# Kernel optimization log

Hardware: AMD Instinct MI355X
Metric: run time of the kernel (lower is better)

## Reference

```python
import math
import jax, jax.numpy as jnp
import numpy as np

B_IN, B_OUT = 32, 16
BATCH, F_IN, F_OUT = 16, 16, 64
N_ALPHA, N_BETA = 8, 4
MAX_BETA = math.pi / 8


def _wigner_d(l, betas):
    """d^l_{m',m}(beta) = <m'|exp(-i beta J_y)|m>, m ordered -l..l (quantum/CS convention)."""
    betas = np.asarray(betas, dtype=np.float64)
    if l == 0:
        return np.ones((len(betas), 1, 1))
    m = np.arange(-l, l)
    c = np.sqrt(l * (l + 1.0) - m * (m + 1.0))
    Jy = np.zeros((2 * l + 1, 2 * l + 1), dtype=np.complex128)
    i = np.arange(2 * l)
    Jy[i + 1, i] = c / 2j
    Jy[i, i + 1] = -c / 2j
    w, V = np.linalg.eigh(Jy)
    ph = np.exp(-1j * betas[:, None] * w[None, :])  # [nb, 2l+1]
    return np.einsum('mk,bk,nk->bmn', V, ph, V.conj()).real


def _quad_weights(b):
    # Driscoll-Healy quadrature weights for the 2b-point SOFT beta grid, incl. alpha weight 2pi/(2b)
    j = np.arange(2 * b)
    beta = np.pi * (2 * j + 1) / (4 * b)
    k = np.arange(b)
    s = np.sum(np.sin(beta[:, None] * (2 * k + 1)[None, :]) / (2 * k + 1)[None, :], axis=1)
    return (2.0 / b) * np.sin(beta) * s * (2.0 * np.pi / (2 * b))


def _tables():
    # S2 forward-FFT table: quadrature-weighted d^l_{m,0}(beta_j)
    betas_in = np.pi * (2 * np.arange(2 * B_IN) + 1) / (4 * B_IN)
    qw = _quad_weights(B_IN)
    nspec = B_OUT ** 2
    wig_s2 = np.zeros((2 * B_IN, nspec))
    for l in range(B_OUT):
        d = _wigner_d(l, betas_in)[:, :, l]  # d^l_{m,0}(beta_j), [2b_in, 2l+1]
        wig_s2[:, l * l:l * l + 2 * l + 1] = d * qw[:, None]
    # kernel spectral basis sampled on the (beta, alpha) grid: e^{-i m alpha} d^l_{m,0}(beta)
    gb = np.repeat((np.arange(N_BETA) + 1) * MAX_BETA / N_BETA, N_ALPHA)
    ga = np.tile(np.linspace(0, 2 * np.pi, N_ALPHA, endpoint=False), N_BETA)
    Fk = np.zeros((nspec, N_ALPHA * N_BETA), dtype=np.complex128)
    for l in range(B_OUT):
        d = _wigner_d(l, gb)[:, :, l]  # [n_grid, 2l+1]
        m = np.arange(-l, l + 1)
        Fk[l * l:l * l + 2 * l + 1] = np.exp(-1j * m[:, None] * ga[None, :]) * d.T
    # SO3 inverse-FFT table: (2l+1) * d^l_{m,n}(beta_k) on the output beta grid
    betas_out = np.pi * (2 * np.arange(2 * B_OUT) + 1) / (4 * B_OUT)
    nspec3 = sum((2 * l + 1) ** 2 for l in range(B_OUT))
    wig_so3 = np.zeros((2 * B_OUT, nspec3))
    off = 0
    for l in range(B_OUT):
        d = _wigner_d(l, betas_out)  # [2b_out, L, L]
        wig_so3[:, off:off + (2 * l + 1) ** 2] = (2 * l + 1) * d.reshape(2 * B_OUT, -1)
        off += (2 * l + 1) ** 2
    return wig_s2, Fk, wig_so3


def setup_inputs() -> dict:
    key = jax.random.key(0)
    kx, kk = jax.random.split(key)
    wig_s2, Fk, wig_so3 = _tables()
    return {
        "x": jax.random.normal(kx, (BATCH, F_IN, 2 * B_IN, 2 * B_IN), dtype=jnp.float32),
        "kernel": jax.random.uniform(kk, (F_IN, F_OUT, N_ALPHA * N_BETA), dtype=jnp.float32, minval=-1.0, maxval=1.0),
        "bias": jnp.zeros((1, F_OUT, 1, 1, 1), dtype=jnp.float32),
        "wig_s2": jnp.asarray(wig_s2, dtype=jnp.float32),
        "fk_re": jnp.asarray(Fk.real, dtype=jnp.float32),
        "fk_im": jnp.asarray(Fk.imag, dtype=jnp.float32),
        "wig_so3": jnp.asarray(wig_so3, dtype=jnp.float32),
    }


def reference(x, kernel, bias, wig_s2, fk_re, fk_im, wig_so3):
    b_in = x.shape[-1] // 2
    nspec = wig_s2.shape[1]
    b_out = int(round(math.sqrt(nspec)))
    batch, f_in = x.shape[0], x.shape[1]
    f_out, n_grid = kernel.shape[1], kernel.shape[2]
    scaling = 1.0 / math.sqrt(n_grid * f_in * b_out ** 4.0 / b_in ** 2.0)

    # --- S2 FFT: FFT over alpha, then quadrature-weighted Legendre (Wigner d_{m0}) sum over beta ---
    xf = jnp.fft.fft(x.astype(jnp.complex64), axis=-1)  # [B, Fin, 2b_in(beta), m-bins]
    m_idx = np.concatenate([np.arange(-l, l + 1) % (2 * b_in) for l in range(b_out)])  # ragged l*m layout
    fhat = jnp.einsum('bfjs,js->sbf', xf[:, :, :, m_idx], wig_s2.astype(jnp.complex64))  # [nspec, B, Fin]

    # --- s2_rft: kernel -> spherical-harmonic coefficients on the sampling grid ---
    Fk = jax.lax.complex(fk_re, fk_im)  # [nspec, n_grid]
    psi = jnp.einsum('iog,sg->sio', (kernel * scaling).astype(jnp.complex64), Fk)  # [nspec, Fin, Fout]

    # --- s2_mm (per-degree ragged block outer product) + SO3 inverse FFT ---
    spec = jnp.zeros((batch, f_out, 2 * b_out, 2 * b_out, 2 * b_out), dtype=jnp.complex64)
    off = 0
    for l in range(b_out):
        L = 2 * l + 1
        s = slice(l * l, l * l + L)
        # Fz^l_{mn} = sum_i fhat^l_m[b,i] * conj(psi^l_n[i,o])
        Fz = jnp.einsum('mbi,nio->bomn', fhat[s], jnp.conj(psi[s]))  # [B, Fout, L, L]
        d_l = wig_so3[:, off:off + L * L].reshape(2 * b_out, L, L).astype(jnp.complex64)
        mi = np.arange(-l, l + 1) % (2 * b_out)
        spec = spec.at[:, :, :, mi[:, None], mi[None, :]].add(
            jnp.einsum('bomn,kmn->bokmn', Fz, d_l))
        off += L * L
    # inverse 2D FFT over (m->alpha, n->gamma); 'forward' norm = unnormalized synthesis sum
    out = jnp.fft.ifft2(spec, axes=(-2, -1), norm='forward').real  # [B, Fout, beta, alpha, gamma]
    return out + bias
```

## Files before the change

### kernel.cpp

```cpp
#include <hip/hip_runtime.h>
#include <math.h>

#define BATCH  16
#define F_IN   16
#define F_OUT  64
#define NGRID  32
#define NSPEC  256
#define NU     136
#define NITEMS 496
#define NP     2856
#define SCALING 0.005524271728019903f
#define PI_F 3.14159265358979323846f
#define W32 0.19634954084936207f

__device__ const int d_cof2[16] = {0,5,22,59,124,225,370,567,824,1149,1550,2035,2612,3289,4074,4975};
__device__ const int d_cumO[16] = {0,16,91,217,386,590,821,1071,1332,1596,1855,2101,2326,2522,2681,2795};

__device__ __forceinline__ void decode_p(int p, int& l, int& m, int& n, int& lam) {
    int L = 0;
    #pragma unroll
    for (int q = 1; q < 16; ++q) if (p >= d_cumO[q]) L = q;
    const int len = 16 - L;
    int q = p - d_cumO[L];
    int ti = (int)((float)q * (1.0f / (float)len));
    int r = q - ti * len;
    if (r < 0) { ti--; r += len; }
    else if (r >= len) { ti++; r -= len; }
    l = L + r;
    lam = L;
    if (ti < 2 * L + 1) { m = L; n = ti - L; }
    else { const int r2 = ti - (2 * L + 1); m = r2 >> 1; n = (r2 & 1) ? L : -L; }
}

__global__ __launch_bounds__(256) void k0_wigt(const float* __restrict__ wig,
                                               float* __restrict__ wigt) {
    const int t = blockIdx.x * 256 + threadIdx.x;
    if (t >= NP * 8) return;
    const int p = t >> 3, kq = t & 7;
    int l, m, n, lam;
    decode_p(p, l, m, n, lam);
    const int wo = d_cof2[l] + m * (2 * l + 1) + n;
    float4 v;
    v.x = wig[(kq * 4 + 0) * 5456 + wo];
    v.y = wig[(kq * 4 + 1) * 5456 + wo];
    v.z = wig[(kq * 4 + 2) * 5456 + wo];
    v.w = wig[(kq * 4 + 3) * 5456 + wo];
    *((float4*)(wigt + ((size_t)kq * NP + p) * 4)) = v;
}

__global__ __launch_bounds__(256) void k1_fhat(const float* __restrict__ x,
                                               const float* __restrict__ wig_s2,
                                               float2* __restrict__ fhat) {
    __shared__ float  xs[64][65];
    __shared__ float2 xf[16][65];
    const int b = blockIdx.x >> 4, f = blockIdx.x & 15;
    const int tid = threadIdx.x;

    const float4* src = (const float4*)(x + (size_t)(b * F_IN + f) * 4096);
    for (int t = tid; t < 1024; t += 256) {
        float4 v = src[t];
        const int row = t >> 4, col = (t & 15) * 4;
        xs[row][col] = v.x; xs[row][col+1] = v.y; xs[row][col+2] = v.z; xs[row][col+3] = v.w;
    }
    __syncthreads();

    {
        const int m = tid >> 4, j0 = tid & 15;
        float stc, sts;
        sincosf(-(2.f * PI_F / 64.f) * (float)m, &sts, &stc);
        float wr = 1.f, wi = 0.f;
        float ar[4] = {0,0,0,0}, ai[4] = {0,0,0,0};
        #pragma unroll 8
        for (int a = 0; a < 64; ++a) {
            #pragma unroll
            for (int q = 0; q < 4; ++q) {
                const float v = xs[j0 + 16*q][a];
                ar[q] += v * wr; ai[q] += v * wi;
            }
            const float nr = wr*stc - wi*sts; wi = wr*sts + wi*stc; wr = nr;
        }
        #pragma unroll
        for (int q = 0; q < 4; ++q) xf[m][j0 + 16*q] = make_float2(ar[q], ai[q]);
    }
    __syncthreads();

    if (tid < NU) {
        int l = (int)((sqrtf(8.f * (float)tid + 1.f) - 1.f) * 0.5f);
        while ((l + 1) * (l + 2) / 2 <= tid) ++l;
        while (l * (l + 1) / 2 > tid) --l;
        const int m = tid - l * (l + 1) / 2;
        const int s = l * l + l + m;
        float re = 0.f, im = 0.f;
        #pragma unroll 8
        for (int j = 0; j < 64; ++j) {
            const float2 v = xf[m][j];
            const float w = wig_s2[j * NSPEC + s];
            re += v.x * w; im += v.y * w;
        }
        fhat[(b * NU + tid) * F_IN + f] = make_float2(re, im);
    }
}

__global__ __launch_bounds__(256) void k2_psic(const float* __restrict__ kern,
                                               const float* __restrict__ fk_re,
                                               const float* __restrict__ fk_im,
                                               float2* __restrict__ psic) {
    __shared__ float2 fk[NGRID];
    const int s = blockIdx.x;
    const int tid = threadIdx.x;
    if (tid < NGRID) fk[tid] = make_float2(fk_re[s * NGRID + tid], -fk_im[s * NGRID + tid]);
    __syncthreads();
    for (int t = tid; t < F_OUT * F_IN; t += 256) {
        const int o = t >> 4, i = t & 15;
        const float* kr = kern + (size_t)(i * F_OUT + o) * NGRID;
        float re = 0.f, im = 0.f;
        for (int g = 0; g < NGRID; ++g) {
            const float v = kr[g];
            re += v * fk[g].x;
            im += v * fk[g].y;
        }
        psic[(o * NSPEC + s) * F_IN + i] = make_float2(re * SCALING, im * SCALING);
    }
}

__global__ __launch_bounds__(256) void k3a_fz(const float2* __restrict__ fhat,
                                              const float2* __restrict__ psic,
                                              float2* __restrict__ fzp) {
    __shared__ __align__(16) float2 fh[NU][18];
    __shared__ __align__(16) float2 ps[NSPEC][18];
    const int bo = blockIdx.x;
    const int b = bo >> 6, o = bo & 63;
    const int tid = threadIdx.x;

    {
        const float2* src = fhat + (size_t)b * NU * F_IN;
        for (int t = tid; t < NU * F_IN; t += 256) fh[t >> 4][t & 15] = src[t];
        const float2* src2 = psic + (size_t)o * NSPEC * F_IN;
        for (int t = tid; t < NSPEC * F_IN; t += 256) ps[t >> 4][t & 15] = src2[t];
    }
    __syncthreads();

    float2* dst = fzp + (size_t)bo * NP;
    for (int p = tid; p < NP; p += 256) {
        int l, m, n, lam;
        decode_p(p, l, m, n, lam);
        const int u = l * (l + 1) / 2 + m;
        const int sn = l * l + l + n;
        const float4* A4 = (const float4*)&fh[u][0];
        const float4* C4 = (const float4*)&ps[sn][0];
        float re = 0.f, im = 0.f;
        #pragma unroll
        for (int i2 = 0; i2 < 8; ++i2) {
            const float4 A = A4[i2], C = C4[i2];
            re += A.x*C.x - A.y*C.y + A.z*C.z - A.w*C.w;
            im += A.x*C.y + A.y*C.x + A.z*C.w + A.w*C.z;
        }
        dst[p] = make_float2(re, im);
    }
}

__global__ __launch_bounds__(256) void k3c_main(const float2* __restrict__ fzp,
                                               const float* __restrict__ wigt,
                                               const float* __restrict__ bias,
                                               float* __restrict__ out) {
    __shared__ __align__(16) float2 S[4][16][33];
    __shared__ __align__(16) float2 G[4][16][33];
    __shared__ float2 tw[32];
    const int bo = blockIdx.x >> 3;
    const int kc = blockIdx.x & 7;
    const int tid = threadIdx.x;
    const float bb = bias[bo & 63];

    if (tid < 32) {
        float s_, c_;
        sincosf(W32 * (float)tid, &s_, &c_);
        tw[tid] = make_float2(c_, s_);
    }

    const float2* fzb = fzp + (size_t)bo * NP;
    const float4* wtb = (const float4*)wigt + (size_t)kc * NP;

    #pragma unroll
    for (int it = 0; it < 2; ++it) {
        const int t = tid + it * 256;
        if (t < NITEMS) {
            int lam = (int)sqrtf((float)t * 0.5f);
            while ((2*lam + 1) * (lam + 1) <= t) ++lam;
            while (lam > 0 && (2*lam - 1) * lam > t) --lam;
            const int r = t - (2*lam - 1) * lam;
            int m, n;
            if (r < 2*lam + 1) { m = lam; n = r - lam; }
            else { const int r2 = r - (2*lam + 1); m = r2 >> 1; n = (r2 & 1) ? lam : -lam; }
            const int len = 16 - lam;
            const int O = d_cumO[lam] + r * len;
            const float2* fz = fzb + O;
            const float4* wt = wtb + O;
            float sr0=0,si0=0,sr1=0,si1=0,sr2=0,si2=0,sr3=0,si3=0;
            for (int j = 0; j < len; ++j) {
                const float2 z = fz[j];
                const float4 w = wt[j];
                sr0 += z.x * w.x; si0 += z.y * w.x;
                sr1 += z.x * w.y; si1 += z.y * w.y;
                sr2 += z.x * w.z; si2 += z.y * w.z;
                sr3 += z.x * w.w; si3 += z.y * w.w;
            }
            const int nn = n + 15;
            S[0][m][nn] = make_float2(sr0, si0);
            S[1][m][nn] = make_float2(sr1, si1);
            S[2][m][nn] = make_float2(sr2, si2);
            S[3][m][nn] = make_float2(sr3, si3);
        }
    }
    __syncthreads();

    {
        const int kk = tid >> 6, m = (tid >> 2) & 15, g0 = tid & 3;
        float ar[4] = {0,0,0,0}, ai[4] = {0,0,0,0}, br[4] = {0,0,0,0}, bi[4] = {0,0,0,0};
        const float2* Srow = &S[kk][m][0];
        #pragma unroll
        for (int nn = 0; nn < 31; ++nn) {
            const float2 sv = Srow[nn];
            const int n = nn - 15;
            #pragma unroll
            for (int q = 0; q < 4; ++q) {
                const int g = g0 + 4 * q;
                const float2 w = tw[(n * g) & 31];
                const float X = sv.x * w.x - sv.y * w.y;
                const float Y = sv.x * w.y + sv.y * w.x;
                ar[q] += X; ai[q] += Y;
                if (nn & 1) { br[q] += X; bi[q] += Y; }
                else        { br[q] -= X; bi[q] -= Y; }
            }
        }
        #pragma unroll
        for (int q = 0; q < 4; ++q) {
            const int g = g0 + 4 * q;
            G[kk][m][g]      = make_float2(ar[q], ai[q]);
            G[kk][m][g + 16] = make_float2(br[q], bi[q]);
        }
    }
    __syncthreads();

    float* outs = (float*)&S[0][0][0];
    {
        const int kk = tid >> 6, g = tid & 31, a0 = (tid >> 5) & 1;
        const float base = G[kk][0][g].x + bb;
        float o_[4][4];
        #pragma unroll
        for (int rep = 0; rep < 4; ++rep)
            #pragma unroll
            for (int j = 0; j < 4; ++j) o_[rep][j] = base;
        #pragma unroll
        for (int m = 1; m < 16; ++m) {
            const float2 gv = G[kk][m][g];
            const float gx = 2.f * gv.x, gy = 2.f * gv.y;
            #pragma unroll
            for (int rep = 0; rep < 4; ++rep) {
                const int A = a0 + 2 * rep;
                const float2 w = tw[(m * A) & 31];
                const float X = gx * w.x - gy * w.y;
                const float Y = gx * w.y + gy * w.x;
                o_[rep][0] += X;
                o_[rep][1] += ((m & 3) == 1) ? -Y : ((m & 3) == 2) ? -X : ((m & 3) == 3) ? Y : X;
                o_[rep][2] += (m & 1) ? -X : X;
                o_[rep][3] += ((m & 3) == 1) ? Y : ((m & 3) == 2) ? -X : ((m & 3) == 3) ? -Y : X;
            }
        }
        #pragma unroll
        for (int rep = 0; rep < 4; ++rep) {
            #pragma unroll
            for (int j = 0; j < 4; ++j) {
                const int a = a0 + 2*rep + 8*j;
                outs[kk * 1024 + (a << 5) + g] = o_[rep][j];
            }
        }
    }
    __syncthreads();

    {
        const int k0 = kc * 4;
        float4* dst = (float4*)(out + (((size_t)bo << 15) + ((size_t)k0 << 10)));
        const float4* s4 = (const float4*)outs;
        #pragma unroll
        for (int it = 0; it < 4; ++it) dst[tid + it * 256] = s4[tid + it * 256];
    }
}

extern "C" void kernel_launch(void* const* d_in, const int* in_sizes, int n_in,
                              void* d_out, int out_size, void* d_ws, size_t ws_size,
                              hipStream_t stream) {
    const float* x       = (const float*)d_in[0];
    const float* kern    = (const float*)d_in[1];
    const float* bias    = (const float*)d_in[2];
    const float* wig_s2  = (const float*)d_in[3];
    const float* fk_re   = (const float*)d_in[4];
    const float* fk_im   = (const float*)d_in[5];
    const float* wig_so3 = (const float*)d_in[6];
    float* out = (float*)d_out;

    float2* fhat_t = (float2*)d_ws;
    float2* psic_t = (float2*)((char*)d_ws + 327680);
    float*  wigt   = (float*)((char*)d_ws + 2424832);
    float2* fzp    = (float2*)((char*)d_ws + 2790400);

    k0_wigt<<<(NP * 8 + 255) / 256, 256, 0, stream>>>(wig_so3, wigt);
    k1_fhat<<<BATCH * F_IN, 256, 0, stream>>>(x, wig_s2, fhat_t);
    k2_psic<<<NSPEC, 256, 0, stream>>>(kern, fk_re, fk_im, psic_t);
    k3a_fz<<<BATCH * F_OUT, 256, 0, stream>>>(fhat_t, psic_t, fzp);
    k3c_main<<<BATCH * F_OUT * 8, 256, 0, stream>>>(fzp, wigt, bias, out);
}
```

Baseline: 352.6 us.

## Merge prep kernels into one launch and halve beta slab per main block

```diff
diff --git a/kernel.cpp b/kernel.cpp
--- a/kernel.cpp
+++ b/kernel.cpp
@@ -32,94 +32,95 @@
     else { const int r2 = ti - (2 * L + 1); m = r2 >> 1; n = (r2 & 1) ? L : -L; }
 }
 
-__global__ __launch_bounds__(256) void k0_wigt(const float* __restrict__ wig,
-                                               float* __restrict__ wigt) {
-    const int t = blockIdx.x * 256 + threadIdx.x;
-    if (t >= NP * 8) return;
-    const int p = t >> 3, kq = t & 7;
-    int l, m, n, lam;
-    decode_p(p, l, m, n, lam);
-    const int wo = d_cof2[l] + m * (2 * l + 1) + n;
-    float4 v;
-    v.x = wig[(kq * 4 + 0) * 5456 + wo];
-    v.y = wig[(kq * 4 + 1) * 5456 + wo];
-    v.z = wig[(kq * 4 + 2) * 5456 + wo];
-    v.w = wig[(kq * 4 + 3) * 5456 + wo];
-    *((float4*)(wigt + ((size_t)kq * NP + p) * 4)) = v;
-}
-
-__global__ __launch_bounds__(256) void k1_fhat(const float* __restrict__ x,
-                                               const float* __restrict__ wig_s2,
-                                               float2* __restrict__ fhat) {
-    __shared__ float  xs[64][65];
-    __shared__ float2 xf[16][65];
-    const int b = blockIdx.x >> 4, f = blockIdx.x & 15;
+__global__ __launch_bounds__(256) void k_prep(const float* __restrict__ x,
+                                              const float* __restrict__ wig_s2,
+                                              const float* __restrict__ kern,
+                                              const float* __restrict__ fk_re,
+                                              const float* __restrict__ fk_im,
+                                              const float* __restrict__ wig,
+                                              float2* __restrict__ fhat,
+                                              float2* __restrict__ psic,
+                                              float2* __restrict__ wigt2) {
+    __shared__ __align__(16) char smem[25088];
+    const int blk = blockIdx.x;
     const int tid = threadIdx.x;
 
-    const float4* src = (const float4*)(x + (size_t)(b * F_IN + f) * 4096);
-    for (int t = tid; t < 1024; t += 256) {
-        float4 v = src[t];
-        const int row = t >> 4, col = (t & 15) * 4;
-        xs[row][col] = v.x; xs[row][col+1] = v.y; xs[row][col+2] = v.z; xs[row][col+3] = v.w;
-    }
-    __syncthreads();
-
-    {
-        const int m = tid >> 4, j0 = tid & 15;
-        float stc, sts;
-        sincosf(-(2.f * PI_F / 64.f) * (float)m, &sts, &stc);
-        float wr = 1.f, wi = 0.f;
-        float ar[4] = {0,0,0,0}, ai[4] = {0,0,0,0};
-        #pragma unroll 8
-        for (int a = 0; a < 64; ++a) {
-            #pragma unroll
-            for (int q = 0; q < 4; ++q) {
-                const float v = xs[j0 + 16*q][a];
-                ar[q] += v * wr; ai[q] += v * wi;
-            }
-            const float nr = wr*stc - wi*sts; wi = wr*sts + wi*stc; wr = nr;
-        }
-        #pragma unroll
-        for (int q = 0; q < 4; ++q) xf[m][j0 + 16*q] = make_float2(ar[q], ai[q]);
-    }
-    __syncthreads();
-
-    if (tid < NU) {
-        int l = (int)((sqrtf(8.f * (float)tid + 1.f) - 1.f) * 0.5f);
-        while ((l + 1) * (l + 2) / 2 <= tid) ++l;
-        while (l * (l + 1) / 2 > tid) --l;
-        const int m = tid - l * (l + 1) / 2;
-        const int s = l * l + l + m;
-        float re = 0.f, im = 0.f;
-        #pragma unroll 8
-        for (int j = 0; j < 64; ++j) {
-            const float2 v = xf[m][j];
-            const float w = wig_s2[j * NSPEC + s];
-            re += v.x * w; im += v.y * w;
-        }
-        fhat[(b * NU + tid) * F_IN + f] = make_float2(re, im);
-    }
-}
-
-__global__ __launch_bounds__(256) void k2_psic(const float* __restrict__ kern,
-                                               const float* __restrict__ fk_re,
-                                               const float* __restrict__ fk_im,
-                                               float2* __restrict__ psic) {
-    __shared__ float2 fk[NGRID];
-    const int s = blockIdx.x;
-    const int tid = threadIdx.x;
-    if (tid < NGRID) fk[tid] = make_float2(fk_re[s * NGRID + tid], -fk_im[s * NGRID + tid]);
-    __syncthreads();
-    for (int t = tid; t < F_OUT * F_IN; t += 256) {
-        const int o = t >> 4, i = t & 15;
-        const float* kr = kern + (size_t)(i * F_OUT + o) * NGRID;
-        float re = 0.f, im = 0.f;
-        for (int g = 0; g < NGRID; ++g) {
-            const float v = kr[g];
-            re += v * fk[g].x;
-            im += v * fk[g].y;
-        }
-        psic[(o * NSPEC + s) * F_IN + i] = make_float2(re * SCALING, im * SCALING);
+    if (blk < 256) {
+        float (*xs)[65]  = (float (*)[65])smem;
+        float2 (*xf)[65] = (float2 (*)[65])(smem + 16640);
+        const int b = blk >> 4, f = blk & 15;
+
+        const float4* src = (const float4*)(x + (size_t)(b * F_IN + f) * 4096);
+        for (int t = tid; t < 1024; t += 256) {
+            float4 v = src[t];
+            const int row = t >> 4, col = (t & 15) * 4;
+            xs[row][col] = v.x; xs[row][col+1] = v.y; xs[row][col+2] = v.z; xs[row][col+3] = v.w;
+        }
+        __syncthreads();
+        {
+            const int m = tid >> 4, j0 = tid & 15;
+            float stc, sts;
+            sincosf(-(2.f * PI_F / 64.f) * (float)m, &sts, &stc);
+            float wr = 1.f, wi = 0.f;
+            float ar[4] = {0,0,0,0}, ai[4] = {0,0,0,0};
+            #pragma unroll 8
+            for (int a = 0; a < 64; ++a) {
+                #pragma unroll
+                for (int q = 0; q < 4; ++q) {
+                    const float v = xs[j0 + 16*q][a];
+                    ar[q] += v * wr; ai[q] += v * wi;
+                }
+                const float nr = wr*stc - wi*sts; wi = wr*sts + wi*stc; wr = nr;
+            }
+            #pragma unroll
+            for (int q = 0; q < 4; ++q) xf[m][j0 + 16*q] = make_float2(ar[q], ai[q]);
+        }
+        __syncthreads();
+        if (tid < NU) {
+            int l = (int)((sqrtf(8.f * (float)tid + 1.f) - 1.f) * 0.5f);
+            while ((l + 1) * (l + 2) / 2 <= tid) ++l;
+            while (l * (l + 1) / 2 > tid) --l;
+            const int m = tid - l * (l + 1) / 2;
+            const int s = l * l + l + m;
+            float re = 0.f, im = 0.f;
+            #pragma unroll 8
+            for (int j = 0; j < 64; ++j) {
+                const float2 v = xf[m][j];
+                const float w = wig_s2[j * NSPEC + s];
+                re += v.x * w; im += v.y * w;
+            }
+            fhat[(b * NU + tid) * F_IN + f] = make_float2(re, im);
+        }
+    } else if (blk < 512) {
+        float2* fk = (float2*)smem;
+        const int s = blk - 256;
+        if (tid < NGRID) fk[tid] = make_float2(fk_re[s * NGRID + tid], -fk_im[s * NGRID + tid]);
+        __syncthreads();
+        for (int t = tid; t < F_OUT * F_IN; t += 256) {
+            const int o = t >> 4, i = t & 15;
+            const float4* kr = (const float4*)(kern + (size_t)(i * F_OUT + o) * NGRID);
+            float re = 0.f, im = 0.f;
+            #pragma unroll
+            for (int g4 = 0; g4 < 8; ++g4) {
+                const float4 v = kr[g4];
+                const float2 a = fk[g4*4+0], b2 = fk[g4*4+1], c = fk[g4*4+2], d = fk[g4*4+3];
+                re += v.x * a.x + v.y * b2.x + v.z * c.x + v.w * d.x;
+                im += v.x * a.y + v.y * b2.y + v.z * c.y + v.w * d.y;
+            }
+            psic[(o * NSPEC + s) * F_IN + i] = make_float2(re * SCALING, im * SCALING);
+        }
+    } else {
+        const int t = (blk - 512) * 256 + tid;
+        if (t < NP * 16) {
+            const int p = t >> 4, kp = t & 15;
+            int l, m, n, lam;
+            decode_p(p, l, m, n, lam);
+            const int wo = d_cof2[l] + m * (2 * l + 1) + n;
+            float2 v;
+            v.x = wig[(2 * kp + 0) * 5456 + wo];
+            v.y = wig[(2 * kp + 1) * 5456 + wo];
+            wigt2[(size_t)kp * NP + p] = v;
+        }
     }
 }
 
@@ -160,14 +161,14 @@
 }
 
 __global__ __launch_bounds__(256) void k3c_main(const float2* __restrict__ fzp,
-                                               const float* __restrict__ wigt,
+                                               const float2* __restrict__ wigt2,
                                                const float* __restrict__ bias,
                                                float* __restrict__ out) {
-    __shared__ __align__(16) float2 S[4][16][33];
-    __shared__ __align__(16) float2 G[4][16][33];
+    __shared__ __align__(16) float2 S[2][16][33];
+    __shared__ __align__(16) float2 G[2][16][33];
     __shared__ float2 tw[32];
-    const int bo = blockIdx.x >> 3;
-    const int kc = blockIdx.x & 7;
+    const int bo = blockIdx.x >> 4;
+    const int kc = blockIdx.x & 15;
     const int tid = threadIdx.x;
     const float bb = bias[bo & 63];
 
@@ -178,7 +179,7 @@
     }
 
     const float2* fzb = fzp + (size_t)bo * NP;
-    const float4* wtb = (const float4*)wigt + (size_t)kc * NP;
+    const float2* wtb = wigt2 + (size_t)kc * NP;
 
     #pragma unroll
     for (int it = 0; it < 2; ++it) {
@@ -194,36 +195,32 @@
             const int len = 16 - lam;
             const int O = d_cumO[lam] + r * len;
             const float2* fz = fzb + O;
-            const float4* wt = wtb + O;
-            float sr0=0,si0=0,sr1=0,si1=0,sr2=0,si2=0,sr3=0,si3=0;
+            const float2* wt = wtb + O;
+            float sr0=0,si0=0,sr1=0,si1=0;
             for (int j = 0; j < len; ++j) {
                 const float2 z = fz[j];
-                const float4 w = wt[j];
+                const float2 w = wt[j];
                 sr0 += z.x * w.x; si0 += z.y * w.x;
                 sr1 += z.x * w.y; si1 += z.y * w.y;
-                sr2 += z.x * w.z; si2 += z.y * w.z;
-                sr3 += z.x * w.w; si3 += z.y * w.w;
             }
             const int nn = n + 15;
             S[0][m][nn] = make_float2(sr0, si0);
             S[1][m][nn] = make_float2(sr1, si1);
-            S[2][m][nn] = make_float2(sr2, si2);
-            S[3][m][nn] = make_float2(sr3, si3);
         }
     }
     __syncthreads();
 
     {
-        const int kk = tid >> 6, m = (tid >> 2) & 15, g0 = tid & 3;
-        float ar[4] = {0,0,0,0}, ai[4] = {0,0,0,0}, br[4] = {0,0,0,0}, bi[4] = {0,0,0,0};
+        const int kk = tid >> 7, m = (tid >> 3) & 15, g0 = tid & 7;
+        float ar[2] = {0,0}, ai[2] = {0,0}, br[2] = {0,0}, bi[2] = {0,0};
         const float2* Srow = &S[kk][m][0];
         #pragma unroll
         for (int nn = 0; nn < 31; ++nn) {
             const float2 sv = Srow[nn];
             const int n = nn - 15;
             #pragma unroll
-            for (int q = 0; q < 4; ++q) {
-                const int g = g0 + 4 * q;
+            for (int q = 0; q < 2; ++q) {
+                const int g = g0 + 8 * q;
                 const float2 w = tw[(n * g) & 31];
                 const float X = sv.x * w.x - sv.y * w.y;
                 const float Y = sv.x * w.y + sv.y * w.x;
@@ -233,8 +230,8 @@
             }
         }
         #pragma unroll
-        for (int q = 0; q < 4; ++q) {
-            const int g = g0 + 4 * q;
+        for (int q = 0; q < 2; ++q) {
+            const int g = g0 + 8 * q;
             G[kk][m][g]      = make_float2(ar[q], ai[q]);
             G[kk][m][g + 16] = make_float2(br[q], bi[q]);
         }
@@ -243,11 +240,11 @@
 
     float* outs = (float*)&S[0][0][0];
     {
-        const int kk = tid >> 6, g = tid & 31, a0 = (tid >> 5) & 1;
+        const int kk = tid >> 7, g = tid & 31, a0 = (tid >> 5) & 3;
         const float base = G[kk][0][g].x + bb;
-        float o_[4][4];
-        #pragma unroll
-        for (int rep = 0; rep < 4; ++rep)
+        float o_[2][4];
+        #pragma unroll
+        for (int rep = 0; rep < 2; ++rep)
             #pragma unroll
             for (int j = 0; j < 4; ++j) o_[rep][j] = base;
         #pragma unroll
@@ -255,8 +252,8 @@
             const float2 gv = G[kk][m][g];
             const float gx = 2.f * gv.x, gy = 2.f * gv.y;
             #pragma unroll
-            for (int rep = 0; rep < 4; ++rep) {
-                const int A = a0 + 2 * rep;
+            for (int rep = 0; rep < 2; ++rep) {
+                const int A = a0 + 4 * rep;
                 const float2 w = tw[(m * A) & 31];
                 const float X = gx * w.x - gy * w.y;
                 const float Y = gx * w.y + gy * w.x;
@@ -267,10 +264,10 @@
             }
         }
         #pragma unroll
-        for (int rep = 0; rep < 4; ++rep) {
+        for (int rep = 0; rep < 2; ++rep) {
             #pragma unroll
             for (int j = 0; j < 4; ++j) {
-                const int a = a0 + 2*rep + 8*j;
+                const int a = a0 + 4*rep + 8*j;
                 outs[kk * 1024 + (a << 5) + g] = o_[rep][j];
             }
         }
@@ -278,11 +275,11 @@
     __syncthreads();
 
     {
-        const int k0 = kc * 4;
+        const int k0 = kc * 2;
         float4* dst = (float4*)(out + (((size_t)bo << 15) + ((size_t)k0 << 10)));
         const float4* s4 = (const float4*)outs;
         #pragma unroll
-        for (int it = 0; it < 4; ++it) dst[tid + it * 256] = s4[tid + it * 256];
+        for (int it = 0; it < 2; ++it) dst[tid + it * 256] = s4[tid + it * 256];
     }
 }
 
@@ -300,12 +297,12 @@
 
     float2* fhat_t = (float2*)d_ws;
     float2* psic_t = (float2*)((char*)d_ws + 327680);
-    float*  wigt   = (float*)((char*)d_ws + 2424832);
+    float2* wigt2  = (float2*)((char*)d_ws + 2424832);
     float2* fzp    = (float2*)((char*)d_ws + 2790400);
 
-    k0_wigt<<<(NP * 8 + 255) / 256, 256, 0, stream>>>(wig_so3, wigt);
-    k1_fhat<<<BATCH * F_IN, 256, 0, stream>>>(x, wig_s2, fhat_t);
-    k2_psic<<<NSPEC, 256, 0, stream>>>(kern, fk_re, fk_im, psic_t);
+    const int prep_blocks = 512 + (NP * 16 + 255) / 256;
+    k_prep<<<prep_blocks, 256, 0, stream>>>(x, wig_s2, kern, fk_re, fk_im, wig_so3,
+                                            fhat_t, psic_t, wigt2);
     k3a_fz<<<BATCH * F_OUT, 256, 0, stream>>>(fhat_t, psic_t, fzp);
-    k3c_main<<<BATCH * F_OUT * 8, 256, 0, stream>>>(fzp, wigt, bias, out);
-}
+    k3c_main<<<BATCH * F_OUT * 16, 256, 0, stream>>>(fzp, wigt2, bias, out);
+}
```

Result: slower. 394.9 us (+12.0%).
